# Kernel tuning notes

Measured on AMD Instinct MI355X. Metric: run time of the kernel, lower is better.

The kernel has to match this reference:

```python
import jax, jax.numpy as jnp
import numpy as np

N = 50000   # nodes
E = 800000  # edges (avg degree 16)
IN = 3      # in_feats = value(1) + u(2)
H = 128     # hid_feats


def setup_inputs() -> dict:
    key = jax.random.key(0)
    ks = jax.random.split(key, 24)
    value = jax.random.normal(ks[0], (N, 1), jnp.float32)
    u = jax.random.normal(ks[1], (N, 2), jnp.float32)
    src = jax.random.randint(ks[2], (E,), 0, N, dtype=jnp.int32)
    dst = jax.random.randint(ks[3], (E,), 0, N, dtype=jnp.int32)
    dims = [IN, H // 2, H, H, H, H, H, H, H, H, 1]
    inp = {"value": value, "u": u, "src": src, "dst": dst}
    for i in range(10):
        inp[f"W{i+1}"] = jax.random.normal(ks[4 + i], (dims[i], dims[i + 1]), jnp.float32) / np.sqrt(dims[i]).astype(np.float32)
        inp[f"b{i+1}"] = jnp.zeros((dims[i + 1],), jnp.float32)
    return inp


def _gconv(x, src, dst, inv_deg, W, b):
    # DGL GraphConv norm='right': sum incoming src features, divide by in-degree, linear, bias
    agg = jax.ops.segment_sum(x[src], dst, num_segments=N)  # [N, d_in]
    return (agg * inv_deg) @ W + b


def reference(value, u, src, dst, W1, b1, W2, b2, W3, b3, W4, b4, W5, b5,
              W6, b6, W7, b7, W8, b8, W9, b9, W10, b10):
    deg = jax.ops.segment_sum(jnp.ones((E,), jnp.float32), dst, num_segments=N)
    inv_deg = (1.0 / jnp.clip(deg, 1.0))[:, None]  # DGL clamps in-degree to >=1
    lrelu = lambda h: jax.nn.leaky_relu(h, 0.01)
    x = jnp.concatenate([value, u], axis=1)  # [N, 3]
    h = _gconv(x, src, dst, inv_deg, W1, b1)
    h = lrelu(_gconv(h, src, dst, inv_deg, W2, b2))
    h = lrelu(_gconv(h, src, dst, inv_deg, W3, b3))
    h = lrelu(_gconv(h, src, dst, inv_deg, W4, b4))
    h = _gconv(h, src, dst, inv_deg, W5, b5)
    h = _gconv(h, src, dst, inv_deg, W6, b6)
    h = _gconv(h, src, dst, inv_deg, W7, b7)
    h = _gconv(h, src, dst, inv_deg, W8, b8)
    h = jax.nn.sigmoid(_gconv(h, src, dst, inv_deg, W9, b9))
    h = _gconv(h, src, dst, inv_deg, W10, b10)  # [N, 1]
    return h
```

## Files before the change

kernel.cpp:

```cpp
#include <hip/hip_runtime.h>
#include <math.h>

typedef unsigned int u32;
typedef unsigned short u16;
using bf16x8 = __attribute__((ext_vector_type(8))) short;
using f32x4 = __attribute__((ext_vector_type(4))) float;

__device__ inline float bf_lo(u32 v) { return __uint_as_float(v << 16); }
__device__ inline float bf_hi(u32 v) { return __uint_as_float(v & 0xFFFF0000u); }
__device__ inline u16 f2bf(float f) {
    u32 u = __float_as_uint(f);
    return (u16)((u + 0x7FFFu + ((u >> 16) & 1u)) >> 16);
}
__device__ inline float bf2f(u16 h) { return __uint_as_float((u32)h << 16); }
__device__ inline float invdeg(int d) { return 1.0f / (float)(d > 1 ? d : 1); }

#define BIN_SHIFT 13

struct W3p { const float* p[3]; };

__global__ __launch_bounds__(256) void k_front(const int* __restrict__ src,
                                               const int* __restrict__ dst,
                                               int* __restrict__ cur,
                                               u16* __restrict__ colp,
                                               int E, int EB, int SB,
                                               const float* __restrict__ value,
                                               const float* __restrict__ u,
                                               float4* __restrict__ x4, int n, int NBx4,
                                               W3p wp,
                                               u16* __restrict__ hi128, u16* __restrict__ lo128) {
    int blk = blockIdx.x;
    if (blk < SB) {
        const int bin = blk / EB;
        int e = (blk - bin * EB) * 256 + threadIdx.x;
        if (e >= E) return;
        int d = dst[e];
        if ((d >> BIN_SHIFT) != bin) return;
        int slot = atomicAdd(&cur[d], 1);
        if (slot < 64) colp[(size_t)d * 64 + slot] = (u16)src[e];
        return;
    }
    int pb = blk - SB;
    if (pb < NBx4) {
        int i = pb * 256 + threadIdx.x;
        if (i < n) x4[i] = make_float4(value[i], u[2 * i], u[2 * i + 1], 1.0f);
        return;
    }
    pb -= NBx4;
    const int l = pb >> 3;
    const float* W = wp.p[l];
    int g = (pb & 7) * 256 + threadIdx.x;
    int ct = g >> 8;
    int rem = g & 255;
    int ks = rem >> 6;
    int lane = rem & 63;
    int kbase = ks * 32 + ((lane >> 4) << 3);
    int nn = (ct << 4) + (lane & 15);
    size_t off = ((size_t)l * 2048 + g) * 8;
#pragma unroll
    for (int j = 0; j < 8; ++j) {
        float w = W[(size_t)(kbase + j) * 128 + nn];
        u16 h = f2bf(w);
        hi128[off + j] = h;
        lo128[off + j] = f2bf(w - bf2f(h));
    }
}

__global__ __launch_bounds__(256) void k_stageA(const float* __restrict__ W7, const float* __restrict__ W8,
                                                const float* __restrict__ b7, const float* __restrict__ b8,
                                                const float* __restrict__ W1, const float* __restrict__ W2,
                                                const float* __restrict__ b1,
                                                float* __restrict__ P1, float* __restrict__ bp1,
                                                float* __restrict__ W12) {
    int blk = blockIdx.x, tid = threadIdx.x;
    if (blk < 64) {
        int idx = blk * 256 + tid;
        int r = idx >> 7, c = idx & 127;
        float s0 = 0.f, s1 = 0.f, s2 = 0.f, s3 = 0.f;
        for (int k = 0; k < 128; k += 4) {
            s0 += W7[r * 128 + k + 0] * W8[(k + 0) * 128 + c];
            s1 += W7[r * 128 + k + 1] * W8[(k + 1) * 128 + c];
            s2 += W7[r * 128 + k + 2] * W8[(k + 2) * 128 + c];
            s3 += W7[r * 128 + k + 3] * W8[(k + 3) * 128 + c];
        }
        P1[idx] = (s0 + s1) + (s2 + s3);
    } else if (blk < 66) {
        int idx = (blk - 64) * 256 + tid;
        if (idx < 384) {
            int r = idx >> 7, c = idx & 127;
            float s = 0.f;
            for (int k = 0; k < 64; ++k) s += W1[r * 64 + k] * W2[k * 128 + c];
            W12[idx] = s;
        }
    } else if (blk == 66) {
        if (tid < 128) {
            float s = 0.f;
            for (int k = 0; k < 64; ++k) s += b1[k] * W2[k * 128 + tid];
            W12[384 + tid] = s;
        }
    } else {
        if (tid < 128) {
            float s = 0.f;
            for (int k = 0; k < 128; ++k) s += b7[k] * W8[k * 128 + tid];
            bp1[tid] = s + b8[tid];
        }
    }
}

__global__ __launch_bounds__(256) void k_stageB(const float* __restrict__ W6,
                                                const float* __restrict__ b6,
                                                const float* __restrict__ P1,
                                                const float* __restrict__ bp1,
                                                float* __restrict__ P2, float* __restrict__ bp2) {
    int blk = blockIdx.x, tid = threadIdx.x;
    if (blk < 64) {
        int idx = blk * 256 + tid;
        int r = idx >> 7, c = idx & 127;
        float s0 = 0.f, s1 = 0.f, s2 = 0.f, s3 = 0.f;
        for (int k = 0; k < 128; k += 4) {
            s0 += W6[r * 128 + k + 0] * P1[(k + 0) * 128 + c];
            s1 += W6[r * 128 + k + 1] * P1[(k + 1) * 128 + c];
            s2 += W6[r * 128 + k + 2] * P1[(k + 2) * 128 + c];
            s3 += W6[r * 128 + k + 3] * P1[(k + 3) * 128 + c];
        }
        P2[idx] = (s0 + s1) + (s2 + s3);
    } else {
        if (tid < 128) {
            float s = 0.f;
            for (int k = 0; k < 128; ++k) s += b6[k] * P1[k * 128 + tid];
            bp2[tid] = s + bp1[tid];
        }
    }
}

__global__ __launch_bounds__(256) void k_stageC(const float* __restrict__ W5,
                                                const float* __restrict__ b5,
                                                const float* __restrict__ P2,
                                                const float* __restrict__ bp2,
                                                u16* __restrict__ pkhi, u16* __restrict__ pklo,
                                                float* __restrict__ bhat) {
    int blk = blockIdx.x, tid = threadIdx.x;
    if (blk < 64) {
        int idx = blk * 256 + tid;
        int k = idx >> 7, c = idx & 127;
        float s0 = 0.f, s1 = 0.f, s2 = 0.f, s3 = 0.f;
        for (int m = 0; m < 128; m += 4) {
            s0 += W5[k * 128 + m + 0] * P2[(m + 0) * 128 + c];
            s1 += W5[k * 128 + m + 1] * P2[(m + 1) * 128 + c];
            s2 += W5[k * 128 + m + 2] * P2[(m + 2) * 128 + c];
            s3 += W5[k * 128 + m + 3] * P2[(m + 3) * 128 + c];
        }
        float val = (s0 + s1) + (s2 + s3);
        u16 h = f2bf(val);
        u16 l = f2bf(val - bf2f(h));
        int lane = (((k >> 3) & 3) << 4) | (c & 15);
        int ct = c >> 4, ks = k >> 5, j = k & 7;
        size_t off = ((size_t)(ct * 4 + ks) * 64 + lane) * 8 + j;
        pkhi[off] = h;
        pklo[off] = l;
    } else {
        if (tid < 128) {
            float s = 0.f;
            for (int k = 0; k < 128; ++k) s += b5[k] * P2[k * 128 + tid];
            bhat[tid] = s + bp2[tid];
        }
    }
}

__global__ __launch_bounds__(256) void k_agg4(const float4* __restrict__ X,
                                              const u16* __restrict__ colp,
                                              const int* __restrict__ deg,
                                              float4* __restrict__ out, int nNodes) {
    int n = blockIdx.x * 256 + threadIdx.x;
    if (n >= nNodes) return;
    int dfull = deg[n];
    int dg = dfull > 64 ? 64 : dfull;
    const u16* cl = colp + (size_t)n * 64;
    float a0 = 0.f, a1 = 0.f, a2 = 0.f, a3 = 0.f;
    int j = 0;
    for (; j + 8 <= dg; j += 8) {
        uint4 q = *reinterpret_cast<const uint4*>(cl + j);
        float4 v0 = X[q.x & 0xFFFFu], v1 = X[q.x >> 16];
        float4 v2 = X[q.y & 0xFFFFu], v3 = X[q.y >> 16];
        float4 v4 = X[q.z & 0xFFFFu], v5 = X[q.z >> 16];
        float4 v6 = X[q.w & 0xFFFFu], v7 = X[q.w >> 16];
        a0 += ((v0.x + v1.x) + (v2.x + v3.x)) + ((v4.x + v5.x) + (v6.x + v7.x));
        a1 += ((v0.y + v1.y) + (v2.y + v3.y)) + ((v4.y + v5.y) + (v6.y + v7.y));
        a2 += ((v0.z + v1.z) + (v2.z + v3.z)) + ((v4.z + v5.z) + (v6.z + v7.z));
        a3 += ((v0.w + v1.w) + (v2.w + v3.w)) + ((v4.w + v5.w) + (v6.w + v7.w));
    }
    for (; j < dg; ++j) {
        float4 v = X[cl[j]];
        a0 += v.x; a1 += v.y; a2 += v.z; a3 += v.w;
    }
    float iv = invdeg(dfull);
    out[n] = make_float4(a0 * iv, a1 * iv, a2 * iv, a3 * iv);
}

template <int ACT>
__device__ inline float actf(float x) {
    if (ACT == 1) return x > 0.f ? x : 0.01f * x;
    if (ACT == 2) return 1.f / (1.f + expf(-x));
    return x;
}

__global__ __launch_bounds__(256) void k_l2(const float4* __restrict__ y2,
                                            const float* __restrict__ W12,
                                            const float* __restrict__ b2,
                                            u16* __restrict__ out, int nNodes) {
    int node = blockIdx.x * 2 + (threadIdx.x >> 7);
    int c = threadIdx.x & 127;
    if (node >= nNodes) return;
    float4 y = y2[node];
    float r = y.x * W12[c] + y.y * W12[128 + c] + y.z * W12[256 + c] + y.w * W12[384 + c] + b2[c];
    out[(size_t)node * 128 + c] = f2bf(actf<1>(r));
}

__global__ __launch_bounds__(256) void k_aggq(const uint4* __restrict__ H4,
                                              const u16* __restrict__ colp,
                                              const int* __restrict__ deg,
                                              uint4* __restrict__ out, int nNodes) {
    const int tid = threadIdx.x;
    const int lane = tid & 63;
    const int wv = tid >> 6;
    const int g = lane >> 4;
    const int c = lane & 15;
    const int n = (blockIdx.x * 4 + wv) * 4 + g;
    const int nn = n < nNodes ? n : nNodes - 1;
    const int dfull = deg[nn];
    const int dg = dfull > 64 ? 64 : dfull;
    const u16* cl = colp + (size_t)nn * 64;

    int dgm = dg;
#pragma unroll
    for (int o = 32; o; o >>= 1) {
        int t = __shfl_xor(dgm, o, 64);
        dgm = t > dgm ? t : dgm;
    }

    float acc0 = 0.f, acc1 = 0.f, acc2 = 0.f, acc3 = 0.f;
    float acc4 = 0.f, acc5 = 0.f, acc6 = 0.f, acc7 = 0.f;

    for (int j = 0; j < dgm; j += 8) {
        uint4 iv4 = *reinterpret_cast<const uint4*>(cl + j);
        int s0 = (int)(iv4.x & 0xFFFFu), s1 = (int)(iv4.x >> 16);
        int s2 = (int)(iv4.y & 0xFFFFu), s3 = (int)(iv4.y >> 16);
        int s4 = (int)(iv4.z & 0xFFFFu), s5 = (int)(iv4.z >> 16);
        int s6 = (int)(iv4.w & 0xFFFFu), s7 = (int)(iv4.w >> 16);
        bool k0 = j + 0 < dg, k1 = j + 1 < dg, k2 = j + 2 < dg, k3 = j + 3 < dg;
        bool k4 = j + 4 < dg, k5 = j + 5 < dg, k6 = j + 6 < dg, k7 = j + 7 < dg;
        if (!k0) s0 = 0; if (!k1) s1 = 0; if (!k2) s2 = 0; if (!k3) s3 = 0;
        if (!k4) s4 = 0; if (!k5) s5 = 0; if (!k6) s6 = 0; if (!k7) s7 = 0;
        uint4 v0 = H4[(size_t)s0 * 16 + c];
        uint4 v1 = H4[(size_t)s1 * 16 + c];
        uint4 v2 = H4[(size_t)s2 * 16 + c];
        uint4 v3 = H4[(size_t)s3 * 16 + c];
        uint4 v4 = H4[(size_t)s4 * 16 + c];
        uint4 v5 = H4[(size_t)s5 * 16 + c];
        uint4 v6 = H4[(size_t)s6 * 16 + c];
        uint4 v7 = H4[(size_t)s7 * 16 + c];
        if (k0) { acc0 += bf_lo(v0.x); acc1 += bf_hi(v0.x); acc2 += bf_lo(v0.y); acc3 += bf_hi(v0.y);
                  acc4 += bf_lo(v0.z); acc5 += bf_hi(v0.z); acc6 += bf_lo(v0.w); acc7 += bf_hi(v0.w); }
        if (k1) { acc0 += bf_lo(v1.x); acc1 += bf_hi(v1.x); acc2 += bf_lo(v1.y); acc3 += bf_hi(v1.y);
                  acc4 += bf_lo(v1.z); acc5 += bf_hi(v1.z); acc6 += bf_lo(v1.w); acc7 += bf_hi(v1.w); }
        if (k2) { acc0 += bf_lo(v2.x); acc1 += bf_hi(v2.x); acc2 += bf_lo(v2.y); acc3 += bf_hi(v2.y);
                  acc4 += bf_lo(v2.z); acc5 += bf_hi(v2.z); acc6 += bf_lo(v2.w); acc7 += bf_hi(v2.w); }
        if (k3) { acc0 += bf_lo(v3.x); acc1 += bf_hi(v3.x); acc2 += bf_lo(v3.y); acc3 += bf_hi(v3.y);
                  acc4 += bf_lo(v3.z); acc5 += bf_hi(v3.z); acc6 += bf_lo(v3.w); acc7 += bf_hi(v3.w); }
        if (k4) { acc0 += bf_lo(v4.x); acc1 += bf_hi(v4.x); acc2 += bf_lo(v4.y); acc3 += bf_hi(v4.y);
                  acc4 += bf_lo(v4.z); acc5 += bf_hi(v4.z); acc6 += bf_lo(v4.w); acc7 += bf_hi(v4.w); }
        if (k5) { acc0 += bf_lo(v5.x); acc1 += bf_hi(v5.x); acc2 += bf_lo(v5.y); acc3 += bf_hi(v5.y);
                  acc4 += bf_lo(v5.z); acc5 += bf_hi(v5.z); acc6 += bf_lo(v5.w); acc7 += bf_hi(v5.w); }
        if (k6) { acc0 += bf_lo(v6.x); acc1 += bf_hi(v6.x); acc2 += bf_lo(v6.y); acc3 += bf_hi(v6.y);
                  acc4 += bf_lo(v6.z); acc5 += bf_hi(v6.z); acc6 += bf_lo(v6.w); acc7 += bf_hi(v6.w); }
        if (k7) { acc0 += bf_lo(v7.x); acc1 += bf_hi(v7.x); acc2 += bf_lo(v7.y); acc3 += bf_hi(v7.y);
                  acc4 += bf_lo(v7.z); acc5 += bf_hi(v7.z); acc6 += bf_lo(v7.w); acc7 += bf_hi(v7.w); }
    }

    float iv = invdeg(dfull);
    uint4 o;
    o.x = (u32)f2bf(acc0 * iv) | ((u32)f2bf(acc1 * iv) << 16);
    o.y = (u32)f2bf(acc2 * iv) | ((u32)f2bf(acc3 * iv) << 16);
    o.z = (u32)f2bf(acc4 * iv) | ((u32)f2bf(acc5 * iv) << 16);
    o.w = (u32)f2bf(acc6 * iv) | ((u32)f2bf(acc7 * iv) << 16);
    if (n < nNodes) out[(size_t)n * 16 + c] = o;
}

template <int ACT>
__global__ __launch_bounds__(256) void k_mm(const u16* __restrict__ A,
                                            const u16* __restrict__ pkHi,
                                            const u16* __restrict__ pkLo,
                                            const float* __restrict__ B,
                                            u16* __restrict__ Y, int nNodes) {
    const int lane = threadIdx.x & 63;
    const int w = threadIdx.x >> 6;
    const int base = blockIdx.x * 64 + w * 16;
    const int m = lane & 15;
    const int kb = lane >> 4;
    int arow = base + m;
    if (arow >= nNodes) arow = nNodes - 1;

    bf16x8 aF[4];
#pragma unroll
    for (int ks = 0; ks < 4; ++ks)
        aF[ks] = *reinterpret_cast<const bf16x8*>(A + (size_t)arow * 128 + ks * 32 + kb * 8);

    const bf16x8* bh = reinterpret_cast<const bf16x8*>(pkHi);
    const bf16x8* bl = reinterpret_cast<const bf16x8*>(pkLo);

#pragma unroll
    for (int ct = 0; ct < 8; ++ct) {
        f32x4 acc = {0.f, 0.f, 0.f, 0.f};
#pragma unroll
        for (int ks = 0; ks < 4; ++ks) {
            acc = __builtin_amdgcn_mfma_f32_16x16x32_bf16(aF[ks], bh[(ct * 4 + ks) * 64 + lane], acc, 0, 0, 0);
            acc = __builtin_amdgcn_mfma_f32_16x16x32_bf16(aF[ks], bl[(ct * 4 + ks) * 64 + lane], acc, 0, 0, 0);
        }
        float bias = B[ct * 16 + m];
#pragma unroll
        for (int r = 0; r < 4; ++r) {
            int row = base + kb * 4 + r;
            if (row < nNodes)
                Y[(size_t)row * 128 + ct * 16 + m] = f2bf(actf<ACT>(acc[r] + bias));
        }
    }
}

__global__ __launch_bounds__(256) void k_mm_last(const u16* __restrict__ A,
                                                 const u16* __restrict__ pkHi,
                                                 const u16* __restrict__ pkLo,
                                                 const float* __restrict__ B,
                                                 const float* __restrict__ w10,
                                                 float* __restrict__ t, int nNodes) {
    const int lane = threadIdx.x & 63;
    const int w = threadIdx.x >> 6;
    const int base = blockIdx.x * 64 + w * 16;
    const int m = lane & 15;
    const int kb = lane >> 4;
    int arow = base + m;
    if (arow >= nNodes) arow = nNodes - 1;

    bf16x8 aF[4];
#pragma unroll
    for (int ks = 0; ks < 4; ++ks)
        aF[ks] = *reinterpret_cast<const bf16x8*>(A + (size_t)arow * 128 + ks * 32 + kb * 8);

    const bf16x8* bh = reinterpret_cast<const bf16x8*>(pkHi);
    const bf16x8* bl = reinterpret_cast<const bf16x8*>(pkLo);

    float p0 = 0.f, p1 = 0.f, p2 = 0.f, p3 = 0.f;
#pragma unroll
    for (int ct = 0; ct < 8; ++ct) {
        f32x4 acc = {0.f, 0.f, 0.f, 0.f};
#pragma unroll
        for (int ks = 0; ks < 4; ++ks) {
            acc = __builtin_amdgcn_mfma_f32_16x16x32_bf16(aF[ks], bh[(ct * 4 + ks) * 64 + lane], acc, 0, 0, 0);
            acc = __builtin_amdgcn_mfma_f32_16x16x32_bf16(aF[ks], bl[(ct * 4 + ks) * 64 + lane], acc, 0, 0, 0);
        }
        float bias = B[ct * 16 + m];
        float wv = w10[ct * 16 + m];
        p0 += wv * actf<2>(acc[0] + bias);
        p1 += wv * actf<2>(acc[1] + bias);
        p2 += wv * actf<2>(acc[2] + bias);
        p3 += wv * actf<2>(acc[3] + bias);
    }
#pragma unroll
    for (int o = 1; o < 16; o <<= 1) {
        p0 += __shfl_xor(p0, o, 64);
        p1 += __shfl_xor(p1, o, 64);
        p2 += __shfl_xor(p2, o, 64);
        p3 += __shfl_xor(p3, o, 64);
    }
    if (m == 0) {
        int r0 = base + kb * 4;
        if (r0 + 0 < nNodes) t[r0 + 0] = p0;
        if (r0 + 1 < nNodes) t[r0 + 1] = p1;
        if (r0 + 2 < nNodes) t[r0 + 2] = p2;
        if (r0 + 3 < nNodes) t[r0 + 3] = p3;
    }
}

__global__ __launch_bounds__(256) void k_aggs(const float* __restrict__ t,
                                              const u16* __restrict__ colp,
                                              const int* __restrict__ deg,
                                              const float* __restrict__ B,
                                              float* __restrict__ out, int nNodes) {
    int n = blockIdx.x * 256 + threadIdx.x;
    if (n >= nNodes) return;
    int dfull = deg[n];
    int dg = dfull > 64 ? 64 : dfull;
    const u16* cl = colp + (size_t)n * 64;
    float s = 0.f;
    for (int j = 0; j < dg; ++j) s += t[cl[j]];
    out[n] = s * invdeg(dfull) + B[0];
}

extern "C" void kernel_launch(void* const* d_in, const int* in_sizes, int n_in,
                              void* d_out, int out_size, void* d_ws, size_t ws_size,
                              hipStream_t stream) {
    const float* value = (const float*)d_in[0];
    const float* u = (const float*)d_in[1];
    const int* src = (const int*)d_in[2];
    const int* dst = (const int*)d_in[3];
    const float* W[10];
    const float* b[10];
    for (int i = 0; i < 10; ++i) {
        W[i] = (const float*)d_in[4 + 2 * i];
        b[i] = (const float*)d_in[5 + 2 * i];
    }
    const int N = in_sizes[0];
    const int E = in_sizes[2];
    float* out = (float*)d_out;

    char* p = (char*)d_ws;
    auto carve = [&](size_t bytes) {
        char* r = p;
        p += (bytes + 255) & ~(size_t)255;
        return r;
    };
    int* deg = (int*)carve((size_t)N * 4);
    u16* colp = (u16*)carve((size_t)N * 64 * 2);
    float4* x4 = (float4*)carve((size_t)N * 16);
    float4* y1 = (float4*)carve((size_t)N * 16);
    float4* y2 = (float4*)carve((size_t)N * 16);
    u16* hA = (u16*)carve((size_t)N * 128 * 2);
    u16* hB = (u16*)carve((size_t)N * 128 * 2);
    u16* agg = (u16*)carve((size_t)N * 128 * 2);
    float* t10 = (float*)carve((size_t)N * 4);
    u16* pkhi = (u16*)carve((size_t)4 * 2048 * 8 * 2);
    u16* pklo = (u16*)carve((size_t)4 * 2048 * 8 * 2);
    float* P1 = (float*)carve((size_t)128 * 128 * 4);
    float* P2 = (float*)carve((size_t)128 * 128 * 4);
    float* bp1 = (float*)carve(128 * 4);
    float* bp2 = (float*)carve(128 * 4);
    float* bhat = (float*)carve(128 * 4);
    float* W12 = (float*)carve(512 * 4);

    const int nbins = (N + (1 << BIN_SHIFT) - 1) >> BIN_SHIFT;
    const int EB = (E + 255) / 256;
    const int SB = EB * nbins;
    const int NBx4 = (N + 255) / 256;

    hipMemsetAsync(deg, 0, (size_t)N * 4, stream);

    W3p wp;
    wp.p[0] = W[2];
    wp.p[1] = W[3];
    wp.p[2] = W[8];
    k_front<<<SB + NBx4 + 24, 256, 0, stream>>>(src, dst, deg, colp, E, EB, SB,
                                                value, u, x4, N, NBx4, wp, pkhi, pklo);
    k_stageA<<<68, 256, 0, stream>>>(W[6], W[7], b[6], b[7], W[0], W[1], b[0], P1, bp1, W12);
    k_stageB<<<65, 256, 0, stream>>>(W[5], b[5], P1, bp1, P2, bp2);
    const size_t PK = 2048 * 8;
    k_stageC<<<65, 256, 0, stream>>>(W[4], b[4], P2, bp2, pkhi + 3 * PK, pklo + 3 * PK, bhat);

    const int ga4 = (N + 255) / 256;
    const int gl2 = (N + 1) / 2;
    const int gq = (N + 15) / 16;
    const int gg = (N + 63) / 64;
    const int gt = (N + 255) / 256;

    k_agg4<<<ga4, 256, 0, stream>>>(x4, colp, deg, y1, N);
    k_agg4<<<ga4, 256, 0, stream>>>(y1, colp, deg, y2, N);
    k_l2<<<gl2, 256, 0, stream>>>(y2, W12, b[1], hA, N);
    k_aggq<<<gq, 256, 0, stream>>>((const uint4*)hA, colp, deg, (uint4*)agg, N);
    k_mm<1><<<gg, 256, 0, stream>>>(agg, pkhi + 0 * PK, pklo + 0 * PK, b[2], hB, N);
    k_aggq<<<gq, 256, 0, stream>>>((const uint4*)hB, colp, deg, (uint4*)agg, N);
    k_mm<1><<<gg, 256, 0, stream>>>(agg, pkhi + 1 * PK, pklo + 1 * PK, b[3], hA, N);
    k_aggq<<<gq, 256, 0, stream>>>((const uint4*)hA, colp, deg, (uint4*)hB, N);
    k_aggq<<<gq, 256, 0, stream>>>((const uint4*)hB, colp, deg, (uint4*)hA, N);
    k_aggq<<<gq, 256, 0, stream>>>((const uint4*)hA, colp, deg, (uint4*)hB, N);
    k_aggq<<<gq, 256, 0, stream>>>((const uint4*)hB, colp, deg, (uint4*)agg, N);
    k_mm<0><<<gg, 256, 0, stream>>>(agg, pkhi + 3 * PK, pklo + 3 * PK, bhat, hA, N);
    k_aggq<<<gq, 256, 0, stream>>>((const uint4*)hA, colp, deg, (uint4*)agg, N);
    k_mm_last<<<gg, 256, 0, stream>>>(agg, pkhi + 2 * PK, pklo + 2 * PK, b[8], W[9], t10, N);
    k_aggs<<<gt, 256, 0, stream>>>(t10, colp, deg, b[9], out, N);
}
```

Baseline: 366.5 us.

## Fold weight-product stages into front kernel and fuse second aggregation with layer-2

The three serial weight-precompute kernels become a reassociated product (W5·W6)·(W7·W8). The two independent products now run inside the front kernel and a single follow-up kernel combines them, cutting two launches and dependency stages. The second 4-wide aggregation is fused with the layer-2 linear+activation, so the y2 buffer and one launch go away. In exchange the fused kernel uses one thread per node writing 128 outputs, which is less parallelism and uses strided per-thread stores.

Measured after the change: 369.8 us. About the same (+0.9%).

```diff
diff --git a/kernel.cpp b/kernel.cpp
--- a/kernel.cpp
+++ b/kernel.cpp
@@ -17,126 +17,122 @@
 
 #define BIN_SHIFT 13
 
-struct W3p { const float* p[3]; };
-
-__global__ __launch_bounds__(256) void k_front(const int* __restrict__ src,
-                                               const int* __restrict__ dst,
-                                               int* __restrict__ cur,
-                                               u16* __restrict__ colp,
-                                               int E, int EB, int SB,
-                                               const float* __restrict__ value,
-                                               const float* __restrict__ u,
-                                               float4* __restrict__ x4, int n, int NBx4,
-                                               W3p wp,
-                                               u16* __restrict__ hi128, u16* __restrict__ lo128) {
+struct FrontArgs {
+    const int *src, *dst;
+    int* cur;
+    u16* colp;
+    int E, EB, SB;
+    const float *value, *uu;
+    float4* x4;
+    int n, NBx4;
+    const float *W3, *W4, *W9;
+    u16 *pkhi, *pklo;
+    const float *W1, *W2, *b1;
+    float* W12;
+    const float *W5, *W6, *W7, *W8, *b5, *b6, *b7, *b8;
+    float *Q1, *Q2, *v, *vw;
+};
+
+__global__ __launch_bounds__(256) void k_front(FrontArgs A) {
     int blk = blockIdx.x;
-    if (blk < SB) {
-        const int bin = blk / EB;
-        int e = (blk - bin * EB) * 256 + threadIdx.x;
-        if (e >= E) return;
-        int d = dst[e];
+    int tid = threadIdx.x;
+    if (blk < A.SB) {
+        const int bin = blk / A.EB;
+        int e = (blk - bin * A.EB) * 256 + tid;
+        if (e >= A.E) return;
+        int d = A.dst[e];
         if ((d >> BIN_SHIFT) != bin) return;
-        int slot = atomicAdd(&cur[d], 1);
-        if (slot < 64) colp[(size_t)d * 64 + slot] = (u16)src[e];
+        int slot = atomicAdd(&A.cur[d], 1);
+        if (slot < 64) A.colp[(size_t)d * 64 + slot] = (u16)A.src[e];
         return;
     }
-    int pb = blk - SB;
-    if (pb < NBx4) {
-        int i = pb * 256 + threadIdx.x;
-        if (i < n) x4[i] = make_float4(value[i], u[2 * i], u[2 * i + 1], 1.0f);
+    int pb = blk - A.SB;
+    if (pb < A.NBx4) {
+        int i = pb * 256 + tid;
+        if (i < A.n) A.x4[i] = make_float4(A.value[i], A.uu[2 * i], A.uu[2 * i + 1], 1.0f);
         return;
     }
-    pb -= NBx4;
-    const int l = pb >> 3;
-    const float* W = wp.p[l];
-    int g = (pb & 7) * 256 + threadIdx.x;
-    int ct = g >> 8;
-    int rem = g & 255;
-    int ks = rem >> 6;
-    int lane = rem & 63;
-    int kbase = ks * 32 + ((lane >> 4) << 3);
-    int nn = (ct << 4) + (lane & 15);
-    size_t off = ((size_t)l * 2048 + g) * 8;
-#pragma unroll
-    for (int j = 0; j < 8; ++j) {
-        float w = W[(size_t)(kbase + j) * 128 + nn];
-        u16 h = f2bf(w);
-        hi128[off + j] = h;
-        lo128[off + j] = f2bf(w - bf2f(h));
-    }
-}
-
-__global__ __launch_bounds__(256) void k_stageA(const float* __restrict__ W7, const float* __restrict__ W8,
-                                                const float* __restrict__ b7, const float* __restrict__ b8,
-                                                const float* __restrict__ W1, const float* __restrict__ W2,
-                                                const float* __restrict__ b1,
-                                                float* __restrict__ P1, float* __restrict__ bp1,
-                                                float* __restrict__ W12) {
-    int blk = blockIdx.x, tid = threadIdx.x;
-    if (blk < 64) {
-        int idx = blk * 256 + tid;
+    pb -= A.NBx4;
+    if (pb < 24) {
+        const float* W = (pb < 8) ? A.W3 : (pb < 16) ? A.W4 : A.W9;
+        const int l = pb >> 3;
+        int g = (pb & 7) * 256 + tid;
+        int ct = g >> 8;
+        int rem = g & 255;
+        int ks = rem >> 6;
+        int lane = rem & 63;
+        int kbase = ks * 32 + ((lane >> 4) << 3);
+        int nn = (ct << 4) + (lane & 15);
+        size_t off = ((size_t)l * 2048 + g) * 8;
+#pragma unroll
+        for (int j = 0; j < 8; ++j) {
+            float w = W[(size_t)(kbase + j) * 128 + nn];
+            u16 h = f2bf(w);
+            A.pkhi[off + j] = h;
+            A.pklo[off + j] = f2bf(w - bf2f(h));
+        }
+        return;
+    }
+    pb -= 24;
+    if (pb < 64) {
+        int idx = pb * 256 + tid;
         int r = idx >> 7, c = idx & 127;
         float s0 = 0.f, s1 = 0.f, s2 = 0.f, s3 = 0.f;
         for (int k = 0; k < 128; k += 4) {
-            s0 += W7[r * 128 + k + 0] * W8[(k + 0) * 128 + c];
-            s1 += W7[r * 128 + k + 1] * W8[(k + 1) * 128 + c];
-            s2 += W7[r * 128 + k + 2] * W8[(k + 2) * 128 + c];
-            s3 += W7[r * 128 + k + 3] * W8[(k + 3) * 128 + c];
-        }
-        P1[idx] = (s0 + s1) + (s2 + s3);
-    } else if (blk < 66) {
-        int idx = (blk - 64) * 256 + tid;
+            s0 += A.W5[r * 128 + k + 0] * A.W6[(k + 0) * 128 + c];
+            s1 += A.W5[r * 128 + k + 1] * A.W6[(k + 1) * 128 + c];
+            s2 += A.W5[r * 128 + k + 2] * A.W6[(k + 2) * 128 + c];
+            s3 += A.W5[r * 128 + k + 3] * A.W6[(k + 3) * 128 + c];
+        }
+        A.Q1[idx] = (s0 + s1) + (s2 + s3);
+        return;
+    }
+    pb -= 64;
+    if (pb < 64) {
+        int idx = pb * 256 + tid;
+        int r = idx >> 7, c = idx & 127;
+        float s0 = 0.f, s1 = 0.f, s2 = 0.f, s3 = 0.f;
+        for (int k = 0; k < 128; k += 4) {
+            s0 += A.W7[r * 128 + k + 0] * A.W8[(k + 0) * 128 + c];
+            s1 += A.W7[r * 128 + k + 1] * A.W8[(k + 1) * 128 + c];
+            s2 += A.W7[r * 128 + k + 2] * A.W8[(k + 2) * 128 + c];
+            s3 += A.W7[r * 128 + k + 3] * A.W8[(k + 3) * 128 + c];
+        }
+        A.Q2[idx] = (s0 + s1) + (s2 + s3);
+        return;
+    }
+    pb -= 64;
+    if (pb < 2) {
+        int idx = pb * 256 + tid;
         if (idx < 384) {
             int r = idx >> 7, c = idx & 127;
             float s = 0.f;
-            for (int k = 0; k < 64; ++k) s += W1[r * 64 + k] * W2[k * 128 + c];
-            W12[idx] = s;
-        }
-    } else if (blk == 66) {
-        if (tid < 128) {
+            for (int k = 0; k < 64; ++k) s += A.W1[r * 64 + k] * A.W2[k * 128 + c];
+            A.W12[idx] = s;
+        } else if (idx < 512) {
+            int c = idx - 384;
             float s = 0.f;
-            for (int k = 0; k < 64; ++k) s += b1[k] * W2[k * 128 + tid];
-            W12[384 + tid] = s;
-        }
+            for (int k = 0; k < 64; ++k) s += A.b1[k] * A.W2[k * 128 + c];
+            A.W12[idx] = s;
+        }
+        return;
+    }
+    if (tid < 128) {
+        float s = 0.f;
+        for (int k = 0; k < 128; ++k) s += A.b5[k] * A.W6[k * 128 + tid];
+        A.v[tid] = s + A.b6[tid];
     } else {
-        if (tid < 128) {
-            float s = 0.f;
-            for (int k = 0; k < 128; ++k) s += b7[k] * W8[k * 128 + tid];
-            bp1[tid] = s + b8[tid];
-        }
-    }
-}
-
-__global__ __launch_bounds__(256) void k_stageB(const float* __restrict__ W6,
-                                                const float* __restrict__ b6,
-                                                const float* __restrict__ P1,
-                                                const float* __restrict__ bp1,
-                                                float* __restrict__ P2, float* __restrict__ bp2) {
-    int blk = blockIdx.x, tid = threadIdx.x;
-    if (blk < 64) {
-        int idx = blk * 256 + tid;
-        int r = idx >> 7, c = idx & 127;
-        float s0 = 0.f, s1 = 0.f, s2 = 0.f, s3 = 0.f;
-        for (int k = 0; k < 128; k += 4) {
-            s0 += W6[r * 128 + k + 0] * P1[(k + 0) * 128 + c];
-            s1 += W6[r * 128 + k + 1] * P1[(k + 1) * 128 + c];
-            s2 += W6[r * 128 + k + 2] * P1[(k + 2) * 128 + c];
-            s3 += W6[r * 128 + k + 3] * P1[(k + 3) * 128 + c];
-        }
-        P2[idx] = (s0 + s1) + (s2 + s3);
-    } else {
-        if (tid < 128) {
-            float s = 0.f;
-            for (int k = 0; k < 128; ++k) s += b6[k] * P1[k * 128 + tid];
-            bp2[tid] = s + bp1[tid];
-        }
-    }
-}
-
-__global__ __launch_bounds__(256) void k_stageC(const float* __restrict__ W5,
-                                                const float* __restrict__ b5,
-                                                const float* __restrict__ P2,
-                                                const float* __restrict__ bp2,
+        int c = tid - 128;
+        float s = 0.f;
+        for (int k = 0; k < 128; ++k) s += A.b7[k] * A.W8[k * 128 + c];
+        A.vw[c] = s + A.b8[c];
+    }
+}
+
+__global__ __launch_bounds__(256) void k_stage2(const float* __restrict__ Q1,
+                                                const float* __restrict__ Q2,
+                                                const float* __restrict__ v,
+                                                const float* __restrict__ vw,
                                                 u16* __restrict__ pkhi, u16* __restrict__ pklo,
                                                 float* __restrict__ bhat) {
     int blk = blockIdx.x, tid = threadIdx.x;
@@ -145,10 +141,10 @@
         int k = idx >> 7, c = idx & 127;
         float s0 = 0.f, s1 = 0.f, s2 = 0.f, s3 = 0.f;
         for (int m = 0; m < 128; m += 4) {
-            s0 += W5[k * 128 + m + 0] * P2[(m + 0) * 128 + c];
-            s1 += W5[k * 128 + m + 1] * P2[(m + 1) * 128 + c];
-            s2 += W5[k * 128 + m + 2] * P2[(m + 2) * 128 + c];
-            s3 += W5[k * 128 + m + 3] * P2[(m + 3) * 128 + c];
+            s0 += Q1[k * 128 + m + 0] * Q2[(m + 0) * 128 + c];
+            s1 += Q1[k * 128 + m + 1] * Q2[(m + 1) * 128 + c];
+            s2 += Q1[k * 128 + m + 2] * Q2[(m + 2) * 128 + c];
+            s3 += Q1[k * 128 + m + 3] * Q2[(m + 3) * 128 + c];
         }
         float val = (s0 + s1) + (s2 + s3);
         u16 h = f2bf(val);
@@ -161,8 +157,8 @@
     } else {
         if (tid < 128) {
             float s = 0.f;
-            for (int k = 0; k < 128; ++k) s += b5[k] * P2[k * 128 + tid];
-            bhat[tid] = s + bp2[tid];
+            for (int k = 0; k < 128; ++k) s += v[k] * Q2[k * 128 + tid];
+            bhat[tid] = s + vw[tid];
         }
     }
 }
@@ -204,16 +200,51 @@
     return x;
 }
 
-__global__ __launch_bounds__(256) void k_l2(const float4* __restrict__ y2,
-                                            const float* __restrict__ W12,
-                                            const float* __restrict__ b2,
-                                            u16* __restrict__ out, int nNodes) {
-    int node = blockIdx.x * 2 + (threadIdx.x >> 7);
-    int c = threadIdx.x & 127;
-    if (node >= nNodes) return;
-    float4 y = y2[node];
-    float r = y.x * W12[c] + y.y * W12[128 + c] + y.z * W12[256 + c] + y.w * W12[384 + c] + b2[c];
-    out[(size_t)node * 128 + c] = f2bf(actf<1>(r));
+__global__ __launch_bounds__(256) void k_agg4l2(const float4* __restrict__ Y1,
+                                                const u16* __restrict__ colp,
+                                                const int* __restrict__ deg,
+                                                const float* __restrict__ W12,
+                                                const float* __restrict__ b2,
+                                                u16* __restrict__ out, int nNodes) {
+    int n = blockIdx.x * 256 + threadIdx.x;
+    if (n >= nNodes) return;
+    int dfull = deg[n];
+    int dg = dfull > 64 ? 64 : dfull;
+    const u16* cl = colp + (size_t)n * 64;
+    float a0 = 0.f, a1 = 0.f, a2 = 0.f, a3 = 0.f;
+    int j = 0;
+    for (; j + 8 <= dg; j += 8) {
+        uint4 q = *reinterpret_cast<const uint4*>(cl + j);
+        float4 v0 = Y1[q.x & 0xFFFFu], v1 = Y1[q.x >> 16];
+        float4 v2 = Y1[q.y & 0xFFFFu], v3 = Y1[q.y >> 16];
+        float4 v4 = Y1[q.z & 0xFFFFu], v5 = Y1[q.z >> 16];
+        float4 v6 = Y1[q.w & 0xFFFFu], v7 = Y1[q.w >> 16];
+        a0 += ((v0.x + v1.x) + (v2.x + v3.x)) + ((v4.x + v5.x) + (v6.x + v7.x));
+        a1 += ((v0.y + v1.y) + (v2.y + v3.y)) + ((v4.y + v5.y) + (v6.y + v7.y));
+        a2 += ((v0.z + v1.z) + (v2.z + v3.z)) + ((v4.z + v5.z) + (v6.z + v7.z));
+        a3 += ((v0.w + v1.w) + (v2.w + v3.w)) + ((v4.w + v5.w) + (v6.w + v7.w));
+    }
+    for (; j < dg; ++j) {
+        float4 v = Y1[cl[j]];
+        a0 += v.x; a1 += v.y; a2 += v.z; a3 += v.w;
+    }
+    float iv = invdeg(dfull);
+    float yx = a0 * iv, yy = a1 * iv, yz = a2 * iv, yw = a3 * iv;
+
+    u16* dst = out + (size_t)n * 128;
+#pragma unroll 4
+    for (int c0 = 0; c0 < 128; c0 += 8) {
+        uint4 o;
+        u32* ow = (u32*)&o;
+#pragma unroll
+        for (int h = 0; h < 4; ++h) {
+            int c = c0 + 2 * h;
+            float r0 = yx * W12[c] + yy * W12[128 + c] + yz * W12[256 + c] + yw * W12[384 + c] + b2[c];
+            float r1 = yx * W12[c + 1] + yy * W12[128 + c + 1] + yz * W12[256 + c + 1] + yw * W12[384 + c + 1] + b2[c + 1];
+            ow[h] = (u32)f2bf(actf<1>(r0)) | ((u32)f2bf(actf<1>(r1)) << 16);
+        }
+        *reinterpret_cast<uint4*>(dst + c0) = o;
+    }
 }
 
 __global__ __launch_bounds__(256) void k_aggq(const uint4* __restrict__ H4,
@@ -422,17 +453,16 @@
     u16* colp = (u16*)carve((size_t)N * 64 * 2);
     float4* x4 = (float4*)carve((size_t)N * 16);
     float4* y1 = (float4*)carve((size_t)N * 16);
-    float4* y2 = (float4*)carve((size_t)N * 16);
     u16* hA = (u16*)carve((size_t)N * 128 * 2);
     u16* hB = (u16*)carve((size_t)N * 128 * 2);
     u16* agg = (u16*)carve((size_t)N * 128 * 2);
     float* t10 = (float*)carve((size_t)N * 4);
     u16* pkhi = (u16*)carve((size_t)4 * 2048 * 8 * 2);
     u16* pklo = (u16*)carve((size_t)4 * 2048 * 8 * 2);
-    float* P1 = (float*)carve((size_t)128 * 128 * 4);
-    float* P2 = (float*)carve((size_t)128 * 128 * 4);
-    float* bp1 = (float*)carve(128 * 4);
-    float* bp2 = (float*)carve(128 * 4);
+    float* Q1 = (float*)carve((size_t)128 * 128 * 4);
+    float* Q2 = (float*)carve((size_t)128 * 128 * 4);
+    float* vv = (float*)carve(128 * 4);
+    float* vw = (float*)carve(128 * 4);
     float* bhat = (float*)carve(128 * 4);
     float* W12 = (float*)carve(512 * 4);
 
@@ -443,26 +473,27 @@
 
     hipMemsetAsync(deg, 0, (size_t)N * 4, stream);
 
-    W3p wp;
-    wp.p[0] = W[2];
-    wp.p[1] = W[3];
-    wp.p[2] = W[8];
-    k_front<<<SB + NBx4 + 24, 256, 0, stream>>>(src, dst, deg, colp, E, EB, SB,
-                                                value, u, x4, N, NBx4, wp, pkhi, pklo);
-    k_stageA<<<68, 256, 0, stream>>>(W[6], W[7], b[6], b[7], W[0], W[1], b[0], P1, bp1, W12);
-    k_stageB<<<65, 256, 0, stream>>>(W[5], b[5], P1, bp1, P2, bp2);
+    FrontArgs FA;
+    FA.src = src; FA.dst = dst; FA.cur = deg; FA.colp = colp;
+    FA.E = E; FA.EB = EB; FA.SB = SB;
+    FA.value = value; FA.uu = u; FA.x4 = x4; FA.n = N; FA.NBx4 = NBx4;
+    FA.W3 = W[2]; FA.W4 = W[3]; FA.W9 = W[8]; FA.pkhi = pkhi; FA.pklo = pklo;
+    FA.W1 = W[0]; FA.W2 = W[1]; FA.b1 = b[0]; FA.W12 = W12;
+    FA.W5 = W[4]; FA.W6 = W[5]; FA.W7 = W[6]; FA.W8 = W[7];
+    FA.b5 = b[4]; FA.b6 = b[5]; FA.b7 = b[6]; FA.b8 = b[7];
+    FA.Q1 = Q1; FA.Q2 = Q2; FA.v = vv; FA.vw = vw;
+    k_front<<<SB + NBx4 + 24 + 64 + 64 + 2 + 1, 256, 0, stream>>>(FA);
+
     const size_t PK = 2048 * 8;
-    k_stageC<<<65, 256, 0, stream>>>(W[4], b[4], P2, bp2, pkhi + 3 * PK, pklo + 3 * PK, bhat);
+    k_stage2<<<65, 256, 0, stream>>>(Q1, Q2, vv, vw, pkhi + 3 * PK, pklo + 3 * PK, bhat);
 
     const int ga4 = (N + 255) / 256;
-    const int gl2 = (N + 1) / 2;
     const int gq = (N + 15) / 16;
     const int gg = (N + 63) / 64;
     const int gt = (N + 255) / 256;
 
     k_agg4<<<ga4, 256, 0, stream>>>(x4, colp, deg, y1, N);
-    k_agg4<<<ga4, 256, 0, stream>>>(y1, colp, deg, y2, N);
-    k_l2<<<gl2, 256, 0, stream>>>(y2, W12, b[1], hA, N);
+    k_agg4l2<<<ga4, 256, 0, stream>>>(y1, colp, deg, W12, b[1], hA, N);
     k_aggq<<<gq, 256, 0, stream>>>((const uint4*)hA, colp, deg, (uint4*)agg, N);
     k_mm<1><<<gg, 256, 0, stream>>>(agg, pkhi + 0 * PK, pklo + 0 * PK, b[2], hB, N);
     k_aggq<<<gq, 256, 0, stream>>>((const uint4*)hB, colp, deg, (uint4*)agg, N);
```
